# Performance work log

Measured on AMD Instinct MI355X. Metric: run time of the kernel, lower is better.

The kernel has to match this reference:

```python
import jax, jax.numpy as jnp
import numpy as np

OUT, IN, GROUP, BITS = 8192, 8192, 128, 4
NG = IN // GROUP  # 64 groups per row

def unpack4(qweight):
    # qweight: [OUT, IN//2] uint8 -> [OUT, IN] int, low nibble first
    low = qweight & jnp.uint8(0x0F)
    high = qweight >> jnp.uint8(4)
    return jnp.stack([low, high], axis=-1).reshape(qweight.shape[0], -1)

def dequantize(qw, scale, zero):
    # qw: [OUT, IN] ints; scale/zero: [OUT, NG]
    q = qw.astype(scale.dtype).reshape(OUT, NG, GROUP)
    w = (q - zero[:, :, None]) * scale[:, :, None]
    return w.reshape(OUT, IN)

def setup_inputs() -> dict:
    key = jax.random.key(0)
    k1, k2, k3, k4 = jax.random.split(key, 4)
    x = jax.random.normal(k1, (8, IN), dtype=jnp.float32)
    qweight = jax.random.randint(k2, (OUT, IN // 2), 0, 256, dtype=jnp.int32).astype(jnp.uint8)
    scale = (jax.random.uniform(k3, (OUT, NG), dtype=jnp.float32) * 0.02 + 0.001)
    zero = jax.random.uniform(k4, (OUT, NG), dtype=jnp.float32) * 15.0
    return {"x": x, "qweight": qweight, "scale": scale, "zero": zero}

def reference(x, qweight, scale, zero):
    w = dequantize(unpack4(qweight), scale, zero)  # [OUT, IN]
    return x @ w.T  # F.linear(x, w), bias=None
```

## Files before the change

kernel.cpp:

```cpp
#include <hip/hip_runtime.h>


typedef __attribute__((ext_vector_type(8))) short bf16x8;
typedef __attribute__((ext_vector_type(4))) float f32x4;

constexpr int Mdim  = 8;
constexpr int N     = 8192;
constexpr int K     = 8192;
constexpr int NG    = 64;
constexpr int KS    = 16;
constexpr int KSL   = K / KS;
constexpr int GPS   = KSL / 128;
constexpr int ROWI4 = K / 8;
constexpr int SLKK  = KSL / 32;

__device__ __forceinline__ float nib_lo(int q) {
    return __int_as_float((q & 15) | 0x4B000000) - 8388608.0f;
}
__device__ __forceinline__ float nib_hi(int q) {
    return __int_as_float(((q >> 4) & 15) | 0x4B000000) - 8388608.0f;
}
__device__ __forceinline__ int pkbf(float lo, float hi) {
    int r;
    asm("v_cvt_pk_bf16_f32 %0, %1, %2" : "=v"(r) : "v"(lo), "v"(hi));
    return r;
}

__device__ __forceinline__ void stage_group(const int4* __restrict__ qw4,
                                            int4* dst, int c0, int kq,
                                            int lane, int g) {
    #pragma unroll
    for (int i = 0; i < 8; ++i) {
        const int rl   = 4 * i + (lane >> 4);
        const int gcol = kq + g * 16 + ((lane & 15) ^ (rl & 15));
        const int4* gp = qw4 + (size_t)(c0 + rl) * ROWI4 + gcol;
        __builtin_amdgcn_global_load_lds(
            (const __attribute__((address_space(1))) void*)gp,
            (__attribute__((address_space(3))) void*)(dst + i * 64),
            16, 0, 0);
    }
}

__global__ __launch_bounds__(256, 2) void qmfma_kernel(
    const float* __restrict__ x,
    const int*   __restrict__ qw,
    const float* __restrict__ scale,
    const float* __restrict__ zero,
    float*       __restrict__ out)
{
    __shared__ int4 As[SLKK * 64];
    __shared__ int4 Bs[4][2][512];

    const int tid  = threadIdx.x;
    const int lane = tid & 63;
    const int wave = tid >> 6;
    const int bid  = blockIdx.x;
    const int ks   = bid >> 6;
    const int nb   = bid & 63;
    const int c0   = nb * 128 + wave * 32;
    const int nl0  = c0 + (lane & 15);
    const int nl1  = nl0 + 16;
    const int kb   = lane >> 4;
    const int r    = lane & 15;

    const int g0 = ks * GPS;
    const int kq = ks * (KSL / 8);

    const int4* __restrict__ qw4 = reinterpret_cast<const int4*>(qw);
    int4 (*BsW)[512] = Bs[wave];

    stage_group(qw4, BsW[0], c0, kq, lane, 0);

    const float4 sv0 = *reinterpret_cast<const float4*>(&scale[nl0 * NG + g0]);
    const float4 zv0 = *reinterpret_cast<const float4*>(&zero [nl0 * NG + g0]);
    const float4 sv1 = *reinterpret_cast<const float4*>(&scale[nl1 * NG + g0]);
    const float4 zv1 = *reinterpret_cast<const float4*>(&zero [nl1 * NG + g0]);
    const float sA0[4] = {sv0.x, sv0.y, sv0.z, sv0.w};
    const float zA0[4] = {zv0.x, zv0.y, zv0.z, zv0.w};
    const float sA1[4] = {sv1.x, sv1.y, sv1.z, sv1.w};
    const float zA1[4] = {zv1.x, zv1.y, zv1.z, zv1.w};

    #pragma unroll
    for (int jf = tid; jf < SLKK * 64; jf += 256) {
        const int ll  = jf & 63;
        const int kk  = jf >> 6;
        const int row = ll & 15;
        const int k0  = ks * KSL + kk * 32 + (ll >> 4) * 8;
        float4 xa = {0.f, 0.f, 0.f, 0.f}, xb = {0.f, 0.f, 0.f, 0.f};
        if (row < Mdim) {
            const float4* xr = reinterpret_cast<const float4*>(x) + (size_t)row * (K / 4);
            xa = xr[k0 / 4];
            xb = xr[k0 / 4 + 1];
        }
        int4 rr;
        rr.x = pkbf(xa.x, xa.y);
        rr.y = pkbf(xa.z, xa.w);
        rr.z = pkbf(xb.x, xb.y);
        rr.w = pkbf(xb.z, xb.w);
        As[jf] = rr;
    }

    asm volatile("s_waitcnt vmcnt(0)" ::: "memory");
    __syncthreads();

    f32x4 acc0 = {0.f, 0.f, 0.f, 0.f};
    f32x4 acc1 = {0.f, 0.f, 0.f, 0.f};

    #pragma unroll
    for (int g = 0; g < GPS; ++g) {
        const int cur = g & 1;
        if (g + 1 < GPS) {
            asm volatile("s_waitcnt lgkmcnt(0)" ::: "memory");
            __builtin_amdgcn_sched_barrier(0);
            stage_group(qw4, BsW[cur ^ 1], c0, kq, lane, g + 1);
            asm volatile("s_waitcnt vmcnt(8)" ::: "memory");
        } else {
            asm volatile("s_waitcnt vmcnt(0)" ::: "memory");
        }
        __builtin_amdgcn_sched_barrier(0);

        const float cs0 = sA0[g], csz0 = zA0[g] * sA0[g];
        const float cs1 = sA1[g], csz1 = zA1[g] * sA1[g];

        #pragma unroll
        for (int t = 0; t < 4; ++t) {
            const int j = t * 4 + kb;
            const int4 qa = BsW[cur][r * 16 + (j ^ r)];
            const int4 qb = BsW[cur][(16 + r) * 16 + (j ^ r)];

            union { int4 u; bf16x8 v; } A, B0, B1;
            A.u = As[(g * 4 + t) * 64 + lane];

            B0.u.x = pkbf(fmaf(nib_lo(qa.x), cs0, -csz0), fmaf(nib_hi(qa.x), cs0, -csz0));
            B0.u.y = pkbf(fmaf(nib_lo(qa.y), cs0, -csz0), fmaf(nib_hi(qa.y), cs0, -csz0));
            B0.u.z = pkbf(fmaf(nib_lo(qa.z), cs0, -csz0), fmaf(nib_hi(qa.z), cs0, -csz0));
            B0.u.w = pkbf(fmaf(nib_lo(qa.w), cs0, -csz0), fmaf(nib_hi(qa.w), cs0, -csz0));
            B1.u.x = pkbf(fmaf(nib_lo(qb.x), cs1, -csz1), fmaf(nib_hi(qb.x), cs1, -csz1));
            B1.u.y = pkbf(fmaf(nib_lo(qb.y), cs1, -csz1), fmaf(nib_hi(qb.y), cs1, -csz1));
            B1.u.z = pkbf(fmaf(nib_lo(qb.z), cs1, -csz1), fmaf(nib_hi(qb.z), cs1, -csz1));
            B1.u.w = pkbf(fmaf(nib_lo(qb.w), cs1, -csz1), fmaf(nib_hi(qb.w), cs1, -csz1));

            acc0 = __builtin_amdgcn_mfma_f32_16x16x32_bf16(A.v, B0.v, acc0, 0, 0, 0);
            acc1 = __builtin_amdgcn_mfma_f32_16x16x32_bf16(A.v, B1.v, acc1, 0, 0, 0);
        }
    }

    if (kb < 2) {
        #pragma unroll
        for (int i = 0; i < 4; ++i) {
            const int m = kb * 4 + i;
            atomicAdd(&out[(size_t)m * N + nl0], acc0[i]);
            atomicAdd(&out[(size_t)m * N + nl1], acc1[i]);
        }
    }
}

extern "C" void kernel_launch(void* const* d_in, const int* in_sizes, int n_in,
                              void* d_out, int out_size, void* d_ws, size_t ws_size,
                              hipStream_t stream) {
    const float* x     = (const float*)d_in[0];
    const int*   qw    = (const int*)d_in[1];
    const float* scale = (const float*)d_in[2];
    const float* zero  = (const float*)d_in[3];
    float*       out   = (float*)d_out;

    hipMemsetAsync(out, 0, (size_t)Mdim * N * sizeof(float), stream);
    qmfma_kernel<<<(N / 128) * KS, 256, 0, stream>>>(x, qw, scale, zero, out);
}
```

Before: 36.31 us.

## Halve per-block column tile and stage whole K-slice up front

```diff
diff --git a/kernel.cpp b/kernel.cpp
--- a/kernel.cpp
+++ b/kernel.cpp
@@ -12,6 +12,7 @@
 constexpr int KSL   = K / KS;
 constexpr int GPS   = KSL / 128;
 constexpr int ROWI4 = K / 8;
+constexpr int SLI4  = KSL / 8;
 constexpr int SLKK  = KSL / 32;
 
 __device__ __forceinline__ float nib_lo(int q) {
@@ -26,21 +27,6 @@
     return r;
 }
 
-__device__ __forceinline__ void stage_group(const int4* __restrict__ qw4,
-                                            int4* dst, int c0, int kq,
-                                            int lane, int g) {
-    #pragma unroll
-    for (int i = 0; i < 8; ++i) {
-        const int rl   = 4 * i + (lane >> 4);
-        const int gcol = kq + g * 16 + ((lane & 15) ^ (rl & 15));
-        const int4* gp = qw4 + (size_t)(c0 + rl) * ROWI4 + gcol;
-        __builtin_amdgcn_global_load_lds(
-            (const __attribute__((address_space(1))) void*)gp,
-            (__attribute__((address_space(3))) void*)(dst + i * 64),
-            16, 0, 0);
-    }
-}
-
 __global__ __launch_bounds__(256, 2) void qmfma_kernel(
     const float* __restrict__ x,
     const int*   __restrict__ qw,
@@ -49,36 +35,38 @@
     float*       __restrict__ out)
 {
     __shared__ int4 As[SLKK * 64];
-    __shared__ int4 Bs[4][2][512];
+    __shared__ int4 Bs[4][16 * SLI4];
 
     const int tid  = threadIdx.x;
     const int lane = tid & 63;
     const int wave = tid >> 6;
     const int bid  = blockIdx.x;
-    const int ks   = bid >> 6;
-    const int nb   = bid & 63;
-    const int c0   = nb * 128 + wave * 32;
-    const int nl0  = c0 + (lane & 15);
-    const int nl1  = nl0 + 16;
+    const int ks   = bid >> 7;
+    const int nb   = bid & 127;
+    const int c0w  = nb * 64 + wave * 16;
+    const int l15  = lane & 15;
     const int kb   = lane >> 4;
-    const int r    = lane & 15;
+    const int nl   = c0w + l15;
 
     const int g0 = ks * GPS;
-    const int kq = ks * (KSL / 8);
+    const int kq = ks * SLI4;
 
     const int4* __restrict__ qw4 = reinterpret_cast<const int4*>(qw);
-    int4 (*BsW)[512] = Bs[wave];
+    int4* BsW = Bs[wave];
 
-    stage_group(qw4, BsW[0], c0, kq, lane, 0);
+    #pragma unroll
+    for (int rr = 0; rr < 16; ++rr) {
+        const int4* gp = qw4 + (size_t)(c0w + rr) * ROWI4 + kq + (lane ^ rr);
+        __builtin_amdgcn_global_load_lds(
+            (const __attribute__((address_space(1))) void*)gp,
+            (__attribute__((address_space(3))) void*)(BsW + rr * SLI4),
+            16, 0, 0);
+    }
 
-    const float4 sv0 = *reinterpret_cast<const float4*>(&scale[nl0 * NG + g0]);
-    const float4 zv0 = *reinterpret_cast<const float4*>(&zero [nl0 * NG + g0]);
-    const float4 sv1 = *reinterpret_cast<const float4*>(&scale[nl1 * NG + g0]);
-    const float4 zv1 = *reinterpret_cast<const float4*>(&zero [nl1 * NG + g0]);
-    const float sA0[4] = {sv0.x, sv0.y, sv0.z, sv0.w};
-    const float zA0[4] = {zv0.x, zv0.y, zv0.z, zv0.w};
-    const float sA1[4] = {sv1.x, sv1.y, sv1.z, sv1.w};
-    const float zA1[4] = {zv1.x, zv1.y, zv1.z, zv1.w};
+    const float4 sv = *reinterpret_cast<const float4*>(&scale[nl * NG + g0]);
+    const float4 zv = *reinterpret_cast<const float4*>(&zero [nl * NG + g0]);
+    const float sA[4] = {sv.x, sv.y, sv.z, sv.w};
+    const float zA[4] = {zv.x, zv.y, zv.z, zv.w};
 
     #pragma unroll
     for (int jf = tid; jf < SLKK * 64; jf += 256) {
@@ -103,45 +91,26 @@
     asm volatile("s_waitcnt vmcnt(0)" ::: "memory");
     __syncthreads();
 
-    f32x4 acc0 = {0.f, 0.f, 0.f, 0.f};
-    f32x4 acc1 = {0.f, 0.f, 0.f, 0.f};
+    f32x4 acc = {0.f, 0.f, 0.f, 0.f};
 
     #pragma unroll
     for (int g = 0; g < GPS; ++g) {
-        const int cur = g & 1;
-        if (g + 1 < GPS) {
-            asm volatile("s_waitcnt lgkmcnt(0)" ::: "memory");
-            __builtin_amdgcn_sched_barrier(0);
-            stage_group(qw4, BsW[cur ^ 1], c0, kq, lane, g + 1);
-            asm volatile("s_waitcnt vmcnt(8)" ::: "memory");
-        } else {
-            asm volatile("s_waitcnt vmcnt(0)" ::: "memory");
-        }
-        __builtin_amdgcn_sched_barrier(0);
-
-        const float cs0 = sA0[g], csz0 = zA0[g] * sA0[g];
-        const float cs1 = sA1[g], csz1 = zA1[g] * sA1[g];
+        const float cs = sA[g], csz = zA[g] * sA[g];
 
         #pragma unroll
         for (int t = 0; t < 4; ++t) {
-            const int j = t * 4 + kb;
-            const int4 qa = BsW[cur][r * 16 + (j ^ r)];
-            const int4 qb = BsW[cur][(16 + r) * 16 + (j ^ r)];
+            const int s = g * 16 + t * 4 + kb;
+            const int4 qa = BsW[l15 * SLI4 + (s ^ l15)];
 
-            union { int4 u; bf16x8 v; } A, B0, B1;
+            union { int4 u; bf16x8 v; } A, B0;
             A.u = As[(g * 4 + t) * 64 + lane];
 
-            B0.u.x = pkbf(fmaf(nib_lo(qa.x), cs0, -csz0), fmaf(nib_hi(qa.x), cs0, -csz0));
-            B0.u.y = pkbf(fmaf(nib_lo(qa.y), cs0, -csz0), fmaf(nib_hi(qa.y), cs0, -csz0));
-            B0.u.z = pkbf(fmaf(nib_lo(qa.z), cs0, -csz0), fmaf(nib_hi(qa.z), cs0, -csz0));
-            B0.u.w = pkbf(fmaf(nib_lo(qa.w), cs0, -csz0), fmaf(nib_hi(qa.w), cs0, -csz0));
-            B1.u.x = pkbf(fmaf(nib_lo(qb.x), cs1, -csz1), fmaf(nib_hi(qb.x), cs1, -csz1));
-            B1.u.y = pkbf(fmaf(nib_lo(qb.y), cs1, -csz1), fmaf(nib_hi(qb.y), cs1, -csz1));
-            B1.u.z = pkbf(fmaf(nib_lo(qb.z), cs1, -csz1), fmaf(nib_hi(qb.z), cs1, -csz1));
-            B1.u.w = pkbf(fmaf(nib_lo(qb.w), cs1, -csz1), fmaf(nib_hi(qb.w), cs1, -csz1));
+            B0.u.x = pkbf(fmaf(nib_lo(qa.x), cs, -csz), fmaf(nib_hi(qa.x), cs, -csz));
+            B0.u.y = pkbf(fmaf(nib_lo(qa.y), cs, -csz), fmaf(nib_hi(qa.y), cs, -csz));
+            B0.u.z = pkbf(fmaf(nib_lo(qa.z), cs, -csz), fmaf(nib_hi(qa.z), cs, -csz));
+            B0.u.w = pkbf(fmaf(nib_lo(qa.w), cs, -csz), fmaf(nib_hi(qa.w), cs, -csz));
 
-            acc0 = __builtin_amdgcn_mfma_f32_16x16x32_bf16(A.v, B0.v, acc0, 0, 0, 0);
-            acc1 = __builtin_amdgcn_mfma_f32_16x16x32_bf16(A.v, B1.v, acc1, 0, 0, 0);
+            acc = __builtin_amdgcn_mfma_f32_16x16x32_bf16(A.v, B0.v, acc, 0, 0, 0);
         }
     }
 
@@ -149,8 +118,7 @@
         #pragma unroll
         for (int i = 0; i < 4; ++i) {
             const int m = kb * 4 + i;
-            atomicAdd(&out[(size_t)m * N + nl0], acc0[i]);
-            atomicAdd(&out[(size_t)m * N + nl1], acc1[i]);
+            atomicAdd(&out[(size_t)m * N + nl], acc[i]);
         }
     }
 }
@@ -165,5 +133,5 @@
     float*       out   = (float*)d_out;
 
     hipMemsetAsync(out, 0, (size_t)Mdim * N * sizeof(float), stream);
-    qmfma_kernel<<<(N / 128) * KS, 256, 0, stream>>>(x, qw, scale, zero, out);
+    qmfma_kernel<<<(N / 64) * KS, 256, 0, stream>>>(x, qw, scale, zero, out);
 }
```

Result: slower. 45.52 us (+25.3%).
